# Optimization experiments

Hardware: AMD Instinct MI355X
Metric: run time of the kernel (lower is better)

The kernel has to match this reference:

```python
import jax, jax.numpy as jnp
import numpy as np

B = 256      # number of graphs
IN = 128     # input_dim
FD = 256     # feature_dim (dims[1])
HID = 256    # hidden_dim of attention block (dims[2])
OUT = 128    # final output dim (dims[3])
TXT = 512    # text_emb_dim

LENGTHS = np.asarray(128 + (np.arange(B) % 256), dtype=np.int64)  # ragged lens 128..383
N = int(LENGTHS.sum())  # 65408 total nodes
LMAX = int(LENGTHS.max())  # 383


def setup_inputs() -> dict:
    key = jax.random.key(0)
    ks = jax.random.split(key, 16)
    s = 0.02
    return {
        "input": jax.random.normal(ks[0], (N, IN), jnp.float32),
        "text_emb": jax.random.normal(ks[1], (B, TXT), jnp.float32),
        "repeat_list": jnp.asarray(LENGTHS),
        # layer 0: Linear(IN -> FD)
        "W0": jax.random.normal(ks[2], (IN, FD), jnp.float32) * s,
        "b0": jax.random.normal(ks[3], (FD,), jnp.float32) * s,
        # cross-attention block params
        "Wq": jax.random.normal(ks[4], (TXT, FD), jnp.float32) * s,
        "bq": jax.random.normal(ks[5], (FD,), jnp.float32) * s,
        "Wk": jax.random.normal(ks[6], (FD, FD), jnp.float32) * s,
        "bk": jax.random.normal(ks[7], (FD,), jnp.float32) * s,
        "Wv": jax.random.normal(ks[8], (FD, FD), jnp.float32) * s,
        "bv": jax.random.normal(ks[9], (FD,), jnp.float32) * s,
        "Wo": jax.random.normal(ks[10], (FD, HID), jnp.float32) * s,
        "bo": jax.random.normal(ks[11], (HID,), jnp.float32) * s,
        # layer 2: Linear(HID -> OUT), last layer (no activation)
        "W2": jax.random.normal(ks[12], (HID, OUT), jnp.float32) * s,
        "b2": jax.random.normal(ks[13], (OUT,), jnp.float32) * s,
    }


def _cross_attention(h, text_emb, repeat_list, Wq, bq, Wk, bk, Wv, bv, Wo, bo):
    # h: [N, FD] packed ragged node features; repeat_list: [B] lengths (constant ints)
    n = h.shape[0]
    b = repeat_list.shape[0]
    fd = h.shape[1]
    # pad ragged -> [B, LMAX, FD] (pad value 0) + validity mask
    seg = jnp.repeat(jnp.arange(b), repeat_list, total_repeat_length=n)  # [N] graph id
    offsets = jnp.cumsum(repeat_list) - repeat_list                      # [B] start of each graph
    pos = jnp.arange(n) - offsets[seg]                                   # [N] within-graph pos
    padded = jnp.zeros((b, LMAX, fd), h.dtype).at[seg, pos].set(h)
    valid = jnp.arange(LMAX)[None, :] < repeat_list[:, None]             # [B, L]

    q = text_emb @ Wq + bq                              # [B, FD]
    k = (padded @ Wk + bk) * valid[..., None]           # masked_fill(mask==0, 0)
    v = (padded @ Wv + bv) * valid[..., None]

    # query is broadcast identically over the padded-length axis, so each row of the
    # [L, L] score matrix is the same vector: scores[b, j] = q[b] . k[b, j]
    scores = jnp.einsum('bf,bjf->bj', q, k)             # [B, L]
    scores = jnp.where(valid, scores, -jnp.inf)         # mask invalid columns j
    p = jax.nn.softmax(scores, axis=-1)                 # [B, L]
    # output = attention^T @ value with identical rows => out[b,j,:] = p[b,j] * sum_i v[b,i,:]
    v_sum = v.sum(axis=1)                               # [B, FD] (padded rows already zero)
    out_pad = p[..., None] * v_sum[:, None, :]          # [B, L, FD]
    out_nodes = out_pad[seg, pos]                       # unpad-concat -> [N, FD]
    return out_nodes @ Wo + bo                          # [N, HID]


def reference(input, text_emb, repeat_list, W0, b0, Wq, bq, Wk, bk, Wv, bv, Wo, bo, W2, b2):
    h = jax.nn.relu(input @ W0 + b0)                                     # layer 0 + relu
    h = _cross_attention(h, text_emb, repeat_list, Wq, bq, Wk, bk, Wv, bv, Wo, bo)
    h = jax.nn.relu(h)                                                   # layer 1 + relu
    return h @ W2 + b2                                                   # layer 2 (last, no act)
```

## Files before the change

### kernel.cpp

```cpp
#include <hip/hip_runtime.h>
#include <math.h>

#define B_G   256
#define IN_D  128
#define FD    256
#define HID   256
#define OUT_D 128
#define TXT   512

typedef short bf16x8 __attribute__((ext_vector_type(8)));
typedef float f32x4  __attribute__((ext_vector_type(4)));

__device__ __forceinline__ unsigned bf_rne(float x) {
    unsigned u = __float_as_uint(x);
    u += 0x7fffu + ((u >> 16) & 1u);
    return u >> 16;
}
__device__ __forceinline__ float bf_to_f(unsigned h) {
    return __uint_as_float(h << 16);
}
__device__ __forceinline__ bf16x8 pack_hi8(const float4& v0, const float4& v1) {
    uint4 h;
    h.x = bf_rne(v0.x) | (bf_rne(v0.y) << 16);
    h.y = bf_rne(v0.z) | (bf_rne(v0.w) << 16);
    h.z = bf_rne(v1.x) | (bf_rne(v1.y) << 16);
    h.w = bf_rne(v1.z) | (bf_rne(v1.w) << 16);
    return __builtin_bit_cast(bf16x8, h);
}

__global__ __launch_bounds__(1024) void k_prepA(
    const float* __restrict__ text_emb, const float* __restrict__ Wq,
    const float* __restrict__ bq, const float* __restrict__ Wk,
    const float* __restrict__ W0, const float* __restrict__ W2,
    const int* __restrict__ lens,
    float* __restrict__ qk, int* __restrict__ offsets, float* __restrict__ hsum,
    unsigned short* __restrict__ W0sH, unsigned short* __restrict__ W0sL,
    unsigned short* __restrict__ W2sH, unsigned short* __restrict__ W2sL)
{
    int blk = blockIdx.x, tid = threadIdx.x;
    int t = tid & 255, g = tid >> 8;
    __shared__ float te[TXT];
    __shared__ float qsh[FD];
    __shared__ float part[4][FD];
    __shared__ int   sc[B_G];

    if (blk < 256) {
        int b = blk;
        if (g == 0) hsum[b * FD + t] = 0.f;
        if (tid < TXT) te[tid] = text_emb[(size_t)b * TXT + tid];
        __syncthreads();
        float acc = (g == 0) ? bq[t] : 0.f;
        const float* Wqp = Wq + (size_t)(128 * g) * FD + t;
        for (int k = 0; k < 128; k++) acc = fmaf(te[128 * g + k], Wqp[(size_t)k * FD], acc);
        part[g][t] = acc;
        __syncthreads();
        if (g == 0) qsh[t] = part[0][t] + part[1][t] + part[2][t] + part[3][t];
        __syncthreads();
        float a2 = 0.f;
        for (int f = 64 * g; f < 64 * g + 64; f++) a2 = fmaf(Wk[(size_t)t * FD + f], qsh[f], a2);
        part[g][t] = a2;
        __syncthreads();
        if (g == 0) qk[b * FD + t] = part[0][t] + part[1][t] + part[2][t] + part[3][t];
    } else if (blk < 258) {
        int e = (blk - 256) * 1024 + tid;
        if (e < 1024) {
            int kc = e >> 8, c = e & 255;
            size_t base = (size_t)(kc * 256 + c) * 32;
            for (int kk = 0; kk < 32; kk++) {
                float v = W0[(size_t)(kc * 32 + kk) * FD + c];
                unsigned h = bf_rne(v);
                float r = v - bf_to_f(h);
                W0sH[base + kk] = (unsigned short)h;
                W0sL[base + kk] = (unsigned short)bf_rne(r);
            }
        } else {
            int e2 = e - 1024;
            int kc = e2 >> 7, c = e2 & 127;
            size_t base = (size_t)(kc * 128 + c) * 32;
            for (int kk = 0; kk < 32; kk++) {
                float v = W2[(size_t)(kc * 32 + kk) * OUT_D + c];
                unsigned h = bf_rne(v);
                float r = v - bf_to_f(h);
                W2sH[base + kk] = (unsigned short)h;
                W2sL[base + kk] = (unsigned short)bf_rne(r);
            }
        }
    } else {
        if (tid < 256) sc[tid] = lens[tid];
        __syncthreads();
        for (int d = 1; d < 256; d <<= 1) {
            int v = (tid < 256 && tid >= d) ? sc[tid - d] : 0;
            __syncthreads();
            if (tid < 256) sc[tid] += v;
            __syncthreads();
        }
        if (tid < 256) offsets[tid + 1] = sc[tid];
        if (tid == 0) offsets[0] = 0;
    }
}

__global__ __launch_bounds__(256, 2) void k_l0_mfma(
    const float* __restrict__ X,
    const unsigned short* __restrict__ W0sH, const unsigned short* __restrict__ W0sL,
    const float* __restrict__ b0, const float* __restrict__ qk,
    const int* __restrict__ offsets,
    float* __restrict__ scores, float* __restrict__ hsum)
{
    int b = blockIdx.y;
    int off = offsets[b], len = offsets[b + 1] - off;
    int n0 = blockIdx.x * 64;
    if (n0 >= len) return;
    int nvalid = min(64, len - n0);

    __shared__ float qks[FD];
    __shared__ float bsh[FD];
    __shared__ float red[4][64];

    int tid = threadIdx.x;
    int lane = tid & 63, w = tid >> 6;
    int ln = lane & 15, quad = lane >> 4;

    qks[tid] = qk[b * FD + tid];
    bsh[tid] = b0[tid];

    const float* Xbase = X + (size_t)(off + n0) * IN_D;
    const float* arow[4];
    bool aval[4];
#pragma unroll
    for (int i = 0; i < 4; i++) {
        int node = 16 * i + ln;
        aval[i] = node < nvalid;
        arow[i] = Xbase + (size_t)(aval[i] ? node : 0) * IN_D + quad * 8;
    }
    const unsigned short* bph[4];
    const unsigned short* bpl[4];
#pragma unroll
    for (int j = 0; j < 4; j++) {
        int c = 64 * w + 16 * j + ln;
        bph[j] = W0sH + (size_t)c * 32 + quad * 8;
        bpl[j] = W0sL + (size_t)c * 32 + quad * 8;
    }

    f32x4 acc[4][4] = {};
    float4 aC[4][2];
#pragma unroll
    for (int i = 0; i < 4; i++) {
        const float4* p = (const float4*)(arow[i]);
        aC[i][0] = p[0]; aC[i][1] = p[1];
    }

#pragma unroll
    for (int kc = 0; kc < 4; kc++) {
        float4 aN[4][2];
        if (kc < 3) {
#pragma unroll
            for (int i = 0; i < 4; i++) {
                const float4* p = (const float4*)(arow[i] + (kc + 1) * 32);
                aN[i][0] = p[0]; aN[i][1] = p[1];
            }
        }
        uint4 bh[4], bl[4];
#pragma unroll
        for (int j = 0; j < 4; j++) {
            bh[j] = *(const uint4*)(bph[j] + (size_t)kc * 8192);
            bl[j] = *(const uint4*)(bpl[j] + (size_t)kc * 8192);
        }
        bf16x8 AH[4];
#pragma unroll
        for (int i = 0; i < 4; i++) {
            float4 v0 = aC[i][0], v1 = aC[i][1];
            if (!aval[i]) { v0 = make_float4(0, 0, 0, 0); v1 = v0; }
            AH[i] = pack_hi8(v0, v1);
        }
#pragma unroll
        for (int i = 0; i < 4; i++)
#pragma unroll
            for (int j = 0; j < 4; j++) {
                acc[i][j] = __builtin_amdgcn_mfma_f32_16x16x32_bf16(
                    AH[i], __builtin_bit_cast(bf16x8, bh[j]), acc[i][j], 0, 0, 0);
                acc[i][j] = __builtin_amdgcn_mfma_f32_16x16x32_bf16(
                    AH[i], __builtin_bit_cast(bf16x8, bl[j]), acc[i][j], 0, 0, 0);
            }
        if (kc < 3) {
#pragma unroll
            for (int i = 0; i < 4; i++) { aC[i][0] = aN[i][0]; aC[i][1] = aN[i][1]; }
        }
    }
    __syncthreads();

    float sp[4][4];
    float cs[4] = {0.f, 0.f, 0.f, 0.f};
#pragma unroll
    for (int i = 0; i < 4; i++)
#pragma unroll
        for (int r = 0; r < 4; r++) sp[i][r] = 0.f;

#pragma unroll
    for (int i = 0; i < 4; i++)
#pragma unroll
        for (int j = 0; j < 4; j++) {
            int c = 64 * w + 16 * j + ln;
            float bb = bsh[c], qv = qks[c];
#pragma unroll
            for (int r = 0; r < 4; r++) {
                int node = 16 * i + 4 * quad + r;
                float h = acc[i][j][r] + bb;
                h = (h > 0.f && node < nvalid) ? h : 0.f;
                sp[i][r] = fmaf(h, qv, sp[i][r]);
                cs[j] += h;
            }
        }
#pragma unroll
    for (int i = 0; i < 4; i++)
#pragma unroll
        for (int r = 0; r < 4; r++) {
            float s = sp[i][r];
            s += __shfl_xor(s, 1); s += __shfl_xor(s, 2);
            s += __shfl_xor(s, 4); s += __shfl_xor(s, 8);
            sp[i][r] = s;
        }
    if (ln == 0) {
#pragma unroll
        for (int i = 0; i < 4; i++)
#pragma unroll
            for (int r = 0; r < 4; r++)
                red[w][16 * i + 4 * quad + r] = sp[i][r];
    }
#pragma unroll
    for (int j = 0; j < 4; j++) {
        float s = cs[j];
        s += __shfl_xor(s, 16); s += __shfl_xor(s, 32);
        if (quad == 0) atomicAdd(&hsum[b * FD + 64 * w + 16 * j + ln], s);
    }
    __syncthreads();
    if (tid < 64 && tid < nvalid)
        scores[off + n0 + tid] = red[0][tid] + red[1][tid] + red[2][tid] + red[3][tid];
}

__global__ __launch_bounds__(1024) void k_graph(
    const float* __restrict__ scores, const float* __restrict__ hsum,
    const float* __restrict__ Wv, const float* __restrict__ bv,
    const float* __restrict__ Wo, const int* __restrict__ offsets,
    float* __restrict__ wvec, float* __restrict__ smax, float* __restrict__ dinv)
{
    int b = blockIdx.x, tid = threadIdx.x;
    int t = tid & 255, g = tid >> 8;
    int off = offsets[b], len = offsets[b + 1] - off;
    __shared__ float redm[16], reds[16];
    __shared__ float hs[FD], vs[FD];
    __shared__ float part[4][FD];

    float m = -INFINITY;
    for (int i = tid; i < len; i += 1024) m = fmaxf(m, scores[off + i]);
    for (int d = 1; d < 64; d <<= 1) m = fmaxf(m, __shfl_xor(m, d));
    if ((tid & 63) == 0) redm[tid >> 6] = m;
    __syncthreads();
    m = -INFINITY;
#pragma unroll
    for (int k = 0; k < 16; k++) m = fmaxf(m, redm[k]);

    float s = 0.f;
    for (int i = tid; i < len; i += 1024) s += expf(scores[off + i] - m);
    for (int d = 1; d < 64; d <<= 1) s += __shfl_xor(s, d);
    if ((tid & 63) == 0) reds[tid >> 6] = s;
    if (g == 0) hs[t] = hsum[b * FD + t];
    __syncthreads();
    s = 0.f;
#pragma unroll
    for (int k = 0; k < 16; k++) s += reds[k];

    float acc = (g == 0) ? (float)len * bv[t] : 0.f;
    for (int f = 64 * g; f < 64 * g + 64; f++) acc = fmaf(hs[f], Wv[f * FD + t], acc);
    part[g][t] = acc;
    __syncthreads();
    if (g == 0) vs[t] = part[0][t] + part[1][t] + part[2][t] + part[3][t];
    __syncthreads();
    float a2 = 0.f;
    for (int f = 64 * g; f < 64 * g + 64; f++) a2 = fmaf(vs[f], Wo[f * HID + t], a2);
    part[g][t] = a2;
    __syncthreads();
    if (g == 0) wvec[b * HID + t] = part[0][t] + part[1][t] + part[2][t] + part[3][t];
    if (tid == 0) { smax[b] = m; dinv[b] = 1.0f / s; }
}

__global__ __launch_bounds__(256, 2) void k_fin_mfma(
    const float* __restrict__ scores, const float* __restrict__ wvec,
    const float* __restrict__ bo,
    const unsigned short* __restrict__ W2sH, const unsigned short* __restrict__ W2sL,
    const float* __restrict__ b2, const float* __restrict__ smax,
    const float* __restrict__ dinv, const int* __restrict__ offsets,
    float* __restrict__ Y)
{
    int b = blockIdx.y;
    int off = offsets[b], len = offsets[b + 1] - off;
    int n0 = blockIdx.x * 64;
    if (n0 >= len) return;
    int nvalid = min(64, len - n0);

    int tid = threadIdx.x;
    int lane = tid & 63, w = tid >> 6;
    int ln = lane & 15, quad = lane >> 4;

    __shared__ float wsh[HID];
    __shared__ float bosh[HID];
    __shared__ float b2sh[OUT_D];

    wsh[tid] = wvec[b * HID + tid];
    bosh[tid] = bo[tid];
    if (tid < OUT_D) b2sh[tid] = b2[tid];

    float sm = smax[b], di = dinv[b];
    float p[4];
#pragma unroll
    for (int i = 0; i < 4; i++) {
        int node = 16 * i + ln;
        p[i] = (node < nvalid) ? expf(scores[off + n0 + node] - sm) * di : 0.f;
    }
    __syncthreads();

    const unsigned short* bph[2];
    const unsigned short* bpl[2];
#pragma unroll
    for (int j = 0; j < 2; j++) {
        int c = 32 * w + 16 * j + ln;
        bph[j] = W2sH + (size_t)c * 32 + quad * 8;
        bpl[j] = W2sL + (size_t)c * 32 + quad * 8;
    }

    f32x4 acc[4][2] = {};
    uint4 bhC[2], blC[2];
#pragma unroll
    for (int j = 0; j < 2; j++) {
        bhC[j] = *(const uint4*)(bph[j]);
        blC[j] = *(const uint4*)(bpl[j]);
    }

#pragma unroll
    for (int kc = 0; kc < 8; kc++) {
        uint4 bhN[2], blN[2];
        if (kc < 7) {
#pragma unroll
            for (int j = 0; j < 2; j++) {
                bhN[j] = *(const uint4*)(bph[j] + (size_t)(kc + 1) * 4096);
                blN[j] = *(const uint4*)(bpl[j] + (size_t)(kc + 1) * 4096);
            }
        }
        float4 wv0 = *(const float4*)&wsh[kc * 32 + quad * 8];
        float4 wv1 = *(const float4*)&wsh[kc * 32 + quad * 8 + 4];
        float4 bo0 = *(const float4*)&bosh[kc * 32 + quad * 8];
        float4 bo1 = *(const float4*)&bosh[kc * 32 + quad * 8 + 4];
        bf16x8 AH[4];
#pragma unroll
        for (int i = 0; i < 4; i++) {
            float4 z0, z1;
            z0.x = fmaxf(fmaf(p[i], wv0.x, bo0.x), 0.f);
            z0.y = fmaxf(fmaf(p[i], wv0.y, bo0.y), 0.f);
            z0.z = fmaxf(fmaf(p[i], wv0.z, bo0.z), 0.f);
            z0.w = fmaxf(fmaf(p[i], wv0.w, bo0.w), 0.f);
            z1.x = fmaxf(fmaf(p[i], wv1.x, bo1.x), 0.f);
            z1.y = fmaxf(fmaf(p[i], wv1.y, bo1.y), 0.f);
            z1.z = fmaxf(fmaf(p[i], wv1.z, bo1.z), 0.f);
            z1.w = fmaxf(fmaf(p[i], wv1.w, bo1.w), 0.f);
            AH[i] = pack_hi8(z0, z1);
        }
#pragma unroll
        for (int i = 0; i < 4; i++)
#pragma unroll
            for (int j = 0; j < 2; j++) {
                acc[i][j] = __builtin_amdgcn_mfma_f32_16x16x32_bf16(
                    AH[i], __builtin_bit_cast(bf16x8, bhC[j]), acc[i][j], 0, 0, 0);
                acc[i][j] = __builtin_amdgcn_mfma_f32_16x16x32_bf16(
                    AH[i], __builtin_bit_cast(bf16x8, blC[j]), acc[i][j], 0, 0, 0);
            }
        if (kc < 7) {
#pragma unroll
            for (int j = 0; j < 2; j++) { bhC[j] = bhN[j]; blC[j] = blN[j]; }
        }
    }

#pragma unroll
    for (int i = 0; i < 4; i++)
#pragma unroll
        for (int j = 0; j < 2; j++) {
            int c = 32 * w + 16 * j + ln;
            float bb = b2sh[c];
#pragma unroll
            for (int r = 0; r < 4; r++) {
                int node = 16 * i + 4 * quad + r;
                if (node < nvalid)
                    Y[(size_t)(off + n0 + node) * OUT_D + c] = acc[i][j][r] + bb;
            }
        }
}

extern "C" void kernel_launch(void* const* d_in, const int* in_sizes, int n_in,
                              void* d_out, int out_size, void* d_ws, size_t ws_size,
                              hipStream_t stream)
{
    const float* X        = (const float*)d_in[0];
    const float* text_emb = (const float*)d_in[1];
    const int*   lens     = (const int*)d_in[2];
    const float* W0       = (const float*)d_in[3];
    const float* b0       = (const float*)d_in[4];
    const float* Wq       = (const float*)d_in[5];
    const float* bq       = (const float*)d_in[6];
    const float* Wk       = (const float*)d_in[7];
    const float* Wv       = (const float*)d_in[9];
    const float* bv       = (const float*)d_in[10];
    const float* Wo       = (const float*)d_in[11];
    const float* bo       = (const float*)d_in[12];
    const float* W2       = (const float*)d_in[13];
    const float* b2       = (const float*)d_in[14];
    float* Y = (float*)d_out;

    char* base = (char*)d_ws;
    size_t o = 0;
    int*   offsets = (int*)(base + o);            o += 1088;
    float* qkbuf   = (float*)(base + o);          o += 262144;
    float* wvec    = (float*)(base + o);          o += 262144;
    float* smaxb   = (float*)(base + o);          o += 1024;
    float* dinvb   = (float*)(base + o);          o += 1024;
    float* hsum    = (float*)(base + o);          o += 262144;
    float* scores  = (float*)(base + o);          o += 262144;
    unsigned short* W0sH = (unsigned short*)(base + o); o += 65536;
    unsigned short* W0sL = (unsigned short*)(base + o); o += 65536;
    unsigned short* W2sH = (unsigned short*)(base + o); o += 65536;
    unsigned short* W2sL = (unsigned short*)(base + o); o += 65536;

    k_prepA<<<259, 1024, 0, stream>>>(text_emb, Wq, bq, Wk, W0, W2, lens,
                                      qkbuf, offsets, hsum, W0sH, W0sL, W2sH, W2sL);
    k_l0_mfma<<<dim3(6, B_G), 256, 0, stream>>>(X, W0sH, W0sL, b0, qkbuf, offsets, scores, hsum);
    k_graph<<<B_G, 1024, 0, stream>>>(scores, hsum, Wv, bv, Wo, offsets, wvec, smaxb, dinvb);
    k_fin_mfma<<<dim3(6, B_G), 256, 0, stream>>>(scores, wvec, bo, W2sH, W2sL, b2, smaxb, dinvb, offsets, Y);
}
```

Baseline: 212.2 us.

## Restructure pipeline into packed 128-node tiles with MFMA q/qk and pre-split weights

Replaces per-graph padded tiling (6 blocks per graph, many partially empty) with dense 128-node tiles over the packed node array. Each tile finds which of at most two graphs it spans by binary search over the offsets. X is pre-converted to bf16 in a prep kernel and staged through LDS. Scores and column sums are accumulated with atomics. The q and qk projections move to split-precision MFMA kernels, and Wq/Wv/Wo are pre-split into bf16 hi/lo. This adds two kernel launches and a full extra read and write of X in bf16, and the 128-row tiling assumes a tile never spans more than two graphs.

```diff
diff --git a/kernel.cpp b/kernel.cpp
--- a/kernel.cpp
+++ b/kernel.cpp
@@ -7,9 +7,15 @@
 #define HID   256
 #define OUT_D 128
 #define TXT   512
+#define NTILES 511
+#define XKS   136
 
 typedef short bf16x8 __attribute__((ext_vector_type(8)));
 typedef float f32x4  __attribute__((ext_vector_type(4)));
+
+__device__ __forceinline__ f32x4 MFMA(bf16x8 a, bf16x8 b, f32x4 c) {
+    return __builtin_amdgcn_mfma_f32_16x16x32_bf16(a, b, c, 0, 0, 0);
+}
 
 __device__ __forceinline__ unsigned bf_rne(float x) {
     unsigned u = __float_as_uint(x);
@@ -27,187 +33,268 @@
     h.w = bf_rne(v1.z) | (bf_rne(v1.w) << 16);
     return __builtin_bit_cast(bf16x8, h);
 }
-
-__global__ __launch_bounds__(1024) void k_prepA(
-    const float* __restrict__ text_emb, const float* __restrict__ Wq,
-    const float* __restrict__ bq, const float* __restrict__ Wk,
-    const float* __restrict__ W0, const float* __restrict__ W2,
+__device__ __forceinline__ void split8hl(const float4& v0, const float4& v1,
+                                         bf16x8& hf, bf16x8& lf) {
+    float a[8] = {v0.x, v0.y, v0.z, v0.w, v1.x, v1.y, v1.z, v1.w};
+    uint4 h, l;
+    unsigned hh[8], ll[8];
+#pragma unroll
+    for (int i = 0; i < 8; i++) {
+        hh[i] = bf_rne(a[i]);
+        ll[i] = bf_rne(a[i] - bf_to_f(hh[i]));
+    }
+    h.x = hh[0] | (hh[1] << 16); h.y = hh[2] | (hh[3] << 16);
+    h.z = hh[4] | (hh[5] << 16); h.w = hh[6] | (hh[7] << 16);
+    l.x = ll[0] | (ll[1] << 16); l.y = ll[2] | (ll[3] << 16);
+    l.z = ll[4] | (ll[5] << 16); l.w = ll[6] | (ll[7] << 16);
+    hf = __builtin_bit_cast(bf16x8, h);
+    lf = __builtin_bit_cast(bf16x8, l);
+}
+
+__device__ __forceinline__ void wsplit(const float* W, int N, int k0, int k1,
+                                       unsigned short* H, unsigned short* L, int c) {
+    if (c >= N) return;
+    for (int k = k0; k < k1; k++) {
+        int kc = k >> 5, kk = k & 31;
+        float v = W[(size_t)k * N + c];
+        unsigned h = bf_rne(v);
+        size_t o = ((size_t)kc * N + c) * 32 + kk;
+        H[o] = (unsigned short)h;
+        L[o] = (unsigned short)bf_rne(v - bf_to_f(h));
+    }
+}
+
+__global__ __launch_bounds__(256) void k_prep(
+    const float* __restrict__ X, const float* __restrict__ W0,
+    const float* __restrict__ W2, const float* __restrict__ Wq,
+    const float* __restrict__ Wv, const float* __restrict__ Wo,
     const int* __restrict__ lens,
-    float* __restrict__ qk, int* __restrict__ offsets, float* __restrict__ hsum,
-    unsigned short* __restrict__ W0sH, unsigned short* __restrict__ W0sL,
-    unsigned short* __restrict__ W2sH, unsigned short* __restrict__ W2sL)
+    unsigned short* __restrict__ Xbf,
+    unsigned short* __restrict__ W0H, unsigned short* __restrict__ W0L,
+    unsigned short* __restrict__ W2H, unsigned short* __restrict__ W2L,
+    unsigned short* __restrict__ WqH, unsigned short* __restrict__ WqL,
+    unsigned short* __restrict__ WvH, unsigned short* __restrict__ WvL,
+    unsigned short* __restrict__ WoH, unsigned short* __restrict__ WoL,
+    int* __restrict__ offsets, float* __restrict__ hsum, float* __restrict__ scores)
 {
     int blk = blockIdx.x, tid = threadIdx.x;
-    int t = tid & 255, g = tid >> 8;
-    __shared__ float te[TXT];
-    __shared__ float qsh[FD];
-    __shared__ float part[4][FD];
-    __shared__ int   sc[B_G];
-
-    if (blk < 256) {
-        int b = blk;
-        if (g == 0) hsum[b * FD + t] = 0.f;
-        if (tid < TXT) te[tid] = text_emb[(size_t)b * TXT + tid];
-        __syncthreads();
-        float acc = (g == 0) ? bq[t] : 0.f;
-        const float* Wqp = Wq + (size_t)(128 * g) * FD + t;
-        for (int k = 0; k < 128; k++) acc = fmaf(te[128 * g + k], Wqp[(size_t)k * FD], acc);
-        part[g][t] = acc;
-        __syncthreads();
-        if (g == 0) qsh[t] = part[0][t] + part[1][t] + part[2][t] + part[3][t];
-        __syncthreads();
-        float a2 = 0.f;
-        for (int f = 64 * g; f < 64 * g + 64; f++) a2 = fmaf(Wk[(size_t)t * FD + f], qsh[f], a2);
-        part[g][t] = a2;
-        __syncthreads();
-        if (g == 0) qk[b * FD + t] = part[0][t] + part[1][t] + part[2][t] + part[3][t];
-    } else if (blk < 258) {
-        int e = (blk - 256) * 1024 + tid;
-        if (e < 1024) {
-            int kc = e >> 8, c = e & 255;
-            size_t base = (size_t)(kc * 256 + c) * 32;
-            for (int kk = 0; kk < 32; kk++) {
-                float v = W0[(size_t)(kc * 32 + kk) * FD + c];
-                unsigned h = bf_rne(v);
-                float r = v - bf_to_f(h);
-                W0sH[base + kk] = (unsigned short)h;
-                W0sL[base + kk] = (unsigned short)bf_rne(r);
-            }
-        } else {
-            int e2 = e - 1024;
-            int kc = e2 >> 7, c = e2 & 127;
-            size_t base = (size_t)(kc * 128 + c) * 32;
-            for (int kk = 0; kk < 32; kk++) {
-                float v = W2[(size_t)(kc * 32 + kk) * OUT_D + c];
-                unsigned h = bf_rne(v);
-                float r = v - bf_to_f(h);
-                W2sH[base + kk] = (unsigned short)h;
-                W2sL[base + kk] = (unsigned short)bf_rne(r);
-            }
-        }
+    if (blk < NTILES) {
+        size_t base = (size_t)blk * 16384;
+#pragma unroll
+        for (int it = 0; it < 8; it++) {
+            size_t off = base + it * 2048 + tid * 8;
+            const float4* p = (const float4*)(X + off);
+            float4 v0 = p[0], v1 = p[1];
+            *(uint4*)(Xbf + off) = __builtin_bit_cast(uint4, pack_hi8(v0, v1));
+        }
+        if (tid < 128) {
+            hsum[blk * 128 + tid] = 0.f;
+            scores[blk * 128 + tid] = 0.f;
+        }
+    } else if (blk == 511) {
+        if (tid < 128) hsum[511 * 128 + tid] = 0.f;
+    } else if (blk == 512) {
+        wsplit(W0, FD, 0, 128, W0H, W0L, tid);
+    } else if (blk == 513) {
+        wsplit(W2, OUT_D, 0, 256, W2H, W2L, tid < 128 ? tid : 9999);
+    } else if (blk == 514) {
+        wsplit(Wq, FD, 0, 256, WqH, WqL, tid);
+    } else if (blk == 515) {
+        wsplit(Wq, FD, 256, 512, WqH, WqL, tid);
+    } else if (blk == 516) {
+        wsplit(Wv, FD, 0, 256, WvH, WvL, tid);
+    } else if (blk == 517) {
+        wsplit(Wo, HID, 0, 256, WoH, WoL, tid);
     } else {
-        if (tid < 256) sc[tid] = lens[tid];
+        __shared__ int sc[B_G];
+        sc[tid] = lens[tid];
         __syncthreads();
         for (int d = 1; d < 256; d <<= 1) {
-            int v = (tid < 256 && tid >= d) ? sc[tid - d] : 0;
+            int v = (tid >= d) ? sc[tid - d] : 0;
             __syncthreads();
-            if (tid < 256) sc[tid] += v;
+            sc[tid] += v;
             __syncthreads();
         }
-        if (tid < 256) offsets[tid + 1] = sc[tid];
+        offsets[tid + 1] = sc[tid];
         if (tid == 0) offsets[0] = 0;
     }
 }
 
-__global__ __launch_bounds__(256, 2) void k_l0_mfma(
-    const float* __restrict__ X,
-    const unsigned short* __restrict__ W0sH, const unsigned short* __restrict__ W0sL,
+__global__ __launch_bounds__(256) void k_q(
+    const float* __restrict__ TE,
+    const unsigned short* __restrict__ WqH, const unsigned short* __restrict__ WqL,
+    const float* __restrict__ bq, float* __restrict__ q)
+{
+    int blk = blockIdx.x;
+    int rbase = (blk >> 2) * 64, cbase = (blk & 3) * 64;
+    int tid = threadIdx.x, lane = tid & 63, w = tid >> 6;
+    int ln = lane & 15, quad = lane >> 4;
+
+    f32x4 acc[4] = {};
+    int arow = rbase + w * 16 + ln;
+#pragma unroll
+    for (int kc = 0; kc < 16; kc++) {
+        const float4* ap = (const float4*)(TE + (size_t)arow * TXT + kc * 32 + quad * 8);
+        bf16x8 AH, AL;
+        split8hl(ap[0], ap[1], AH, AL);
+#pragma unroll
+        for (int j = 0; j < 4; j++) {
+            int c = cbase + 16 * j + ln;
+            size_t bo = ((size_t)kc * 256 + c) * 32 + quad * 8;
+            bf16x8 BH = *(const bf16x8*)(WqH + bo);
+            bf16x8 BL = *(const bf16x8*)(WqL + bo);
+            acc[j] = MFMA(AH, BH, acc[j]);
+            acc[j] = MFMA(AH, BL, acc[j]);
+            acc[j] = MFMA(AL, BH, acc[j]);
+        }
+    }
+#pragma unroll
+    for (int j = 0; j < 4; j++) {
+        int c = cbase + 16 * j + ln;
+        float bb = bq[c];
+#pragma unroll
+        for (int r = 0; r < 4; r++) {
+            int row = rbase + w * 16 + quad * 4 + r;
+            q[(size_t)row * FD + c] = acc[j][r] + bb;
+        }
+    }
+}
+
+__global__ __launch_bounds__(256) void k_qk(
+    const float* __restrict__ q, const float* __restrict__ Wk,
+    float* __restrict__ qk)
+{
+    int blk = blockIdx.x;
+    int rbase = (blk >> 2) * 64, cbase = (blk & 3) * 64;
+    int tid = threadIdx.x, lane = tid & 63, w = tid >> 6;
+    int ln = lane & 15, quad = lane >> 4;
+
+    f32x4 acc[4] = {};
+    int arow = rbase + w * 16 + ln;
+#pragma unroll
+    for (int kc = 0; kc < 8; kc++) {
+        const float4* ap = (const float4*)(q + (size_t)arow * FD + kc * 32 + quad * 8);
+        bf16x8 AH, AL;
+        split8hl(ap[0], ap[1], AH, AL);
+#pragma unroll
+        for (int j = 0; j < 4; j++) {
+            int f = cbase + 16 * j + ln;
+            const float4* bp = (const float4*)(Wk + (size_t)f * FD + kc * 32 + quad * 8);
+            bf16x8 BH, BL;
+            split8hl(bp[0], bp[1], BH, BL);
+            acc[j] = MFMA(AH, BH, acc[j]);
+            acc[j] = MFMA(AH, BL, acc[j]);
+            acc[j] = MFMA(AL, BH, acc[j]);
+        }
+    }
+#pragma unroll
+    for (int j = 0; j < 4; j++) {
+        int f = cbase + 16 * j + ln;
+#pragma unroll
+        for (int r = 0; r < 4; r++) {
+            int row = rbase + w * 16 + quad * 4 + r;
+            qk[(size_t)row * FD + f] = acc[j][r];
+        }
+    }
+}
+
+__global__ __launch_bounds__(256) void k_l0(
+    const unsigned short* __restrict__ Xbf,
+    const unsigned short* __restrict__ W0H, const unsigned short* __restrict__ W0L,
     const float* __restrict__ b0, const float* __restrict__ qk,
     const int* __restrict__ offsets,
     float* __restrict__ scores, float* __restrict__ hsum)
 {
-    int b = blockIdx.y;
-    int off = offsets[b], len = offsets[b + 1] - off;
-    int n0 = blockIdx.x * 64;
-    if (n0 >= len) return;
-    int nvalid = min(64, len - n0);
-
-    __shared__ float qks[FD];
-    __shared__ float bsh[FD];
-    __shared__ float red[4][64];
-
-    int tid = threadIdx.x;
-    int lane = tid & 63, w = tid >> 6;
+    int t = blockIdx.y, bx = blockIdx.x;
+    int n0 = t * 128;
+    int tid = threadIdx.x, lane = tid & 63, w = tid >> 6;
     int ln = lane & 15, quad = lane >> 4;
-
-    qks[tid] = qk[b * FD + tid];
-    bsh[tid] = b0[tid];
-
-    const float* Xbase = X + (size_t)(off + n0) * IN_D;
-    const float* arow[4];
-    bool aval[4];
-#pragma unroll
-    for (int i = 0; i < 4; i++) {
-        int node = 16 * i + ln;
-        aval[i] = node < nvalid;
-        arow[i] = Xbase + (size_t)(aval[i] ? node : 0) * IN_D + quad * 8;
-    }
-    const unsigned short* bph[4];
-    const unsigned short* bpl[4];
-#pragma unroll
-    for (int j = 0; j < 4; j++) {
-        int c = 64 * w + 16 * j + ln;
-        bph[j] = W0sH + (size_t)c * 32 + quad * 8;
-        bpl[j] = W0sL + (size_t)c * 32 + quad * 8;
-    }
+    int i2 = w & 1, j2 = w >> 1;
+
+    __shared__ __align__(16) unsigned short Xs[128 * XKS];
+    __shared__ int offs[257];
+    __shared__ float qks[2][128];
+    __shared__ float bsh[128];
+
+    offs[tid] = offsets[tid];
+    if (tid == 0) offs[256] = offsets[256];
+    __syncthreads();
+
+    int lo = 0, hi = 255;
+#pragma unroll
+    for (int s = 0; s < 8; s++) {
+        int mid = (lo + hi + 1) >> 1;
+        if (offs[mid] <= n0) lo = mid; else hi = mid - 1;
+    }
+    int g0 = lo;
+    lo = g0; hi = 255;
+#pragma unroll
+    for (int s = 0; s < 8; s++) {
+        int mid = (lo + hi + 1) >> 1;
+        if (offs[mid] <= n0 + 127) lo = mid; else hi = mid - 1;
+    }
+    int g1 = lo;
+    int boundary = (g1 > g0) ? offs[g1] : 0x7fffffff;
+
+    if (tid < 128) {
+        bsh[tid] = b0[bx * 128 + tid];
+        qks[0][tid] = qk[(size_t)g0 * FD + bx * 128 + tid];
+        qks[1][tid] = qk[(size_t)g1 * FD + bx * 128 + tid];
+    }
+#pragma unroll
+    for (int it = 0; it < 8; it++) {
+        int row = it * 16 + (tid >> 4);
+        int kq = (tid & 15) * 8;
+        *(uint4*)(Xs + row * XKS + kq) =
+            *(const uint4*)(Xbf + (size_t)(n0 + row) * IN_D + kq);
+    }
+    __syncthreads();
 
     f32x4 acc[4][4] = {};
-    float4 aC[4][2];
-#pragma unroll
-    for (int i = 0; i < 4; i++) {
-        const float4* p = (const float4*)(arow[i]);
-        aC[i][0] = p[0]; aC[i][1] = p[1];
-    }
-
 #pragma unroll
     for (int kc = 0; kc < 4; kc++) {
-        float4 aN[4][2];
-        if (kc < 3) {
-#pragma unroll
-            for (int i = 0; i < 4; i++) {
-                const float4* p = (const float4*)(arow[i] + (kc + 1) * 32);
-                aN[i][0] = p[0]; aN[i][1] = p[1];
-            }
-        }
-        uint4 bh[4], bl[4];
+        bf16x8 AH[4], BH[4], BL[4];
+#pragma unroll
+        for (int i = 0; i < 4; i++)
+            AH[i] = *(const bf16x8*)(Xs + (i2 * 64 + 16 * i + ln) * XKS + kc * 32 + quad * 8);
 #pragma unroll
         for (int j = 0; j < 4; j++) {
-            bh[j] = *(const uint4*)(bph[j] + (size_t)kc * 8192);
-            bl[j] = *(const uint4*)(bpl[j] + (size_t)kc * 8192);
-        }
-        bf16x8 AH[4];
-#pragma unroll
-        for (int i = 0; i < 4; i++) {
-            float4 v0 = aC[i][0], v1 = aC[i][1];
-            if (!aval[i]) { v0 = make_float4(0, 0, 0, 0); v1 = v0; }
-            AH[i] = pack_hi8(v0, v1);
+            int c = bx * 128 + j2 * 64 + 16 * j + ln;
+            size_t bo = ((size_t)kc * 256 + c) * 32 + quad * 8;
+            BH[j] = *(const bf16x8*)(W0H + bo);
+            BL[j] = *(const bf16x8*)(W0L + bo);
         }
 #pragma unroll
         for (int i = 0; i < 4; i++)
 #pragma unroll
             for (int j = 0; j < 4; j++) {
-                acc[i][j] = __builtin_amdgcn_mfma_f32_16x16x32_bf16(
-                    AH[i], __builtin_bit_cast(bf16x8, bh[j]), acc[i][j], 0, 0, 0);
-                acc[i][j] = __builtin_amdgcn_mfma_f32_16x16x32_bf16(
-                    AH[i], __builtin_bit_cast(bf16x8, bl[j]), acc[i][j], 0, 0, 0);
-            }
-        if (kc < 3) {
-#pragma unroll
-            for (int i = 0; i < 4; i++) { aC[i][0] = aN[i][0]; aC[i][1] = aN[i][1]; }
-        }
-    }
-    __syncthreads();
+                acc[i][j] = MFMA(AH[i], BH[j], acc[i][j]);
+                acc[i][j] = MFMA(AH[i], BL[j], acc[i][j]);
+            }
+    }
 
     float sp[4][4];
-    float cs[4] = {0.f, 0.f, 0.f, 0.f};
+    float cs[4][2];
 #pragma unroll
     for (int i = 0; i < 4; i++)
 #pragma unroll
         for (int r = 0; r < 4; r++) sp[i][r] = 0.f;
+#pragma unroll
+    for (int j = 0; j < 4; j++) { cs[j][0] = 0.f; cs[j][1] = 0.f; }
 
 #pragma unroll
     for (int i = 0; i < 4; i++)
 #pragma unroll
         for (int j = 0; j < 4; j++) {
-            int c = 64 * w + 16 * j + ln;
-            float bb = bsh[c], qv = qks[c];
+            int cl = j2 * 64 + 16 * j + ln;
+            float bb = bsh[cl];
 #pragma unroll
             for (int r = 0; r < 4; r++) {
-                int node = 16 * i + 4 * quad + r;
-                float h = acc[i][j][r] + bb;
-                h = (h > 0.f && node < nvalid) ? h : 0.f;
-                sp[i][r] = fmaf(h, qv, sp[i][r]);
-                cs[j] += h;
+                int node = i2 * 64 + 16 * i + quad * 4 + r;
+                int gb = (n0 + node >= boundary) ? 1 : 0;
+                float h = fmaxf(acc[i][j][r] + bb, 0.f);
+                sp[i][r] = fmaf(h, qks[gb][cl], sp[i][r]);
+                cs[j][gb] += h;
             }
         }
 #pragma unroll
@@ -217,141 +304,209 @@
             float s = sp[i][r];
             s += __shfl_xor(s, 1); s += __shfl_xor(s, 2);
             s += __shfl_xor(s, 4); s += __shfl_xor(s, 8);
-            sp[i][r] = s;
-        }
-    if (ln == 0) {
-#pragma unroll
-        for (int i = 0; i < 4; i++)
-#pragma unroll
-            for (int r = 0; r < 4; r++)
-                red[w][16 * i + 4 * quad + r] = sp[i][r];
-    }
+            if (ln == 0) {
+                int node = i2 * 64 + 16 * i + quad * 4 + r;
+                atomicAdd(&scores[n0 + node], s);
+            }
+        }
 #pragma unroll
     for (int j = 0; j < 4; j++) {
-        float s = cs[j];
-        s += __shfl_xor(s, 16); s += __shfl_xor(s, 32);
-        if (quad == 0) atomicAdd(&hsum[b * FD + 64 * w + 16 * j + ln], s);
-    }
-    __syncthreads();
-    if (tid < 64 && tid < nvalid)
-        scores[off + n0 + tid] = red[0][tid] + red[1][tid] + red[2][tid] + red[3][tid];
-}
-
-__global__ __launch_bounds__(1024) void k_graph(
+        int cl = j2 * 64 + 16 * j + ln;
+#pragma unroll
+        for (int gb = 0; gb < 2; gb++) {
+            float s = cs[j][gb];
+            s += __shfl_xor(s, 16); s += __shfl_xor(s, 32);
+            if (quad == 0 && (gb == 0 || g1 > g0)) {
+                int g = gb ? g1 : g0;
+                atomicAdd(&hsum[(size_t)g * FD + bx * 128 + cl], s);
+            }
+        }
+    }
+}
+
+__global__ __launch_bounds__(256) void k_mid(
     const float* __restrict__ scores, const float* __restrict__ hsum,
-    const float* __restrict__ Wv, const float* __restrict__ bv,
-    const float* __restrict__ Wo, const int* __restrict__ offsets,
+    const unsigned short* __restrict__ WvH, const unsigned short* __restrict__ WvL,
+    const float* __restrict__ bv,
+    const unsigned short* __restrict__ WoH, const unsigned short* __restrict__ WoL,
+    const int* __restrict__ offsets,
     float* __restrict__ wvec, float* __restrict__ smax, float* __restrict__ dinv)
 {
-    int b = blockIdx.x, tid = threadIdx.x;
-    int t = tid & 255, g = tid >> 8;
-    int off = offsets[b], len = offsets[b + 1] - off;
-    __shared__ float redm[16], reds[16];
-    __shared__ float hs[FD], vs[FD];
-    __shared__ float part[4][FD];
-
-    float m = -INFINITY;
-    for (int i = tid; i < len; i += 1024) m = fmaxf(m, scores[off + i]);
-    for (int d = 1; d < 64; d <<= 1) m = fmaxf(m, __shfl_xor(m, d));
-    if ((tid & 63) == 0) redm[tid >> 6] = m;
-    __syncthreads();
-    m = -INFINITY;
-#pragma unroll
-    for (int k = 0; k < 16; k++) m = fmaxf(m, redm[k]);
-
-    float s = 0.f;
-    for (int i = tid; i < len; i += 1024) s += expf(scores[off + i] - m);
-    for (int d = 1; d < 64; d <<= 1) s += __shfl_xor(s, d);
-    if ((tid & 63) == 0) reds[tid >> 6] = s;
-    if (g == 0) hs[t] = hsum[b * FD + t];
-    __syncthreads();
-    s = 0.f;
-#pragma unroll
-    for (int k = 0; k < 16; k++) s += reds[k];
-
-    float acc = (g == 0) ? (float)len * bv[t] : 0.f;
-    for (int f = 64 * g; f < 64 * g + 64; f++) acc = fmaf(hs[f], Wv[f * FD + t], acc);
-    part[g][t] = acc;
-    __syncthreads();
-    if (g == 0) vs[t] = part[0][t] + part[1][t] + part[2][t] + part[3][t];
-    __syncthreads();
-    float a2 = 0.f;
-    for (int f = 64 * g; f < 64 * g + 64; f++) a2 = fmaf(vs[f], Wo[f * HID + t], a2);
-    part[g][t] = a2;
-    __syncthreads();
-    if (g == 0) wvec[b * HID + t] = part[0][t] + part[1][t] + part[2][t] + part[3][t];
-    if (tid == 0) { smax[b] = m; dinv[b] = 1.0f / s; }
-}
-
-__global__ __launch_bounds__(256, 2) void k_fin_mfma(
+    int blk = blockIdx.x, tid = threadIdx.x;
+    if (blk < 4) {
+        __shared__ float vs[64 * 260];
+        __shared__ int offs2[65];
+        int base = blk * 64;
+        int lane = tid & 63, w = tid >> 6;
+        int ln = lane & 15, quad = lane >> 4;
+        if (tid < 65) offs2[tid] = offsets[base + tid];
+        __syncthreads();
+
+        f32x4 acc[4][4] = {};
+#pragma unroll
+        for (int kc = 0; kc < 8; kc++) {
+            bf16x8 AH[4], AL[4], BH[4], BL[4];
+#pragma unroll
+            for (int i = 0; i < 4; i++) {
+                const float4* ap = (const float4*)(hsum + (size_t)(base + 16 * i + ln) * FD + kc * 32 + quad * 8);
+                split8hl(ap[0], ap[1], AH[i], AL[i]);
+            }
+#pragma unroll
+            for (int j = 0; j < 4; j++) {
+                int c = w * 64 + 16 * j + ln;
+                size_t bo = ((size_t)kc * 256 + c) * 32 + quad * 8;
+                BH[j] = *(const bf16x8*)(WvH + bo);
+                BL[j] = *(const bf16x8*)(WvL + bo);
+            }
+#pragma unroll
+            for (int i = 0; i < 4; i++)
+#pragma unroll
+                for (int j = 0; j < 4; j++) {
+                    acc[i][j] = MFMA(AH[i], BH[j], acc[i][j]);
+                    acc[i][j] = MFMA(AH[i], BL[j], acc[i][j]);
+                    acc[i][j] = MFMA(AL[i], BH[j], acc[i][j]);
+                }
+        }
+#pragma unroll
+        for (int i = 0; i < 4; i++)
+#pragma unroll
+            for (int j = 0; j < 4; j++) {
+                int c = w * 64 + 16 * j + ln;
+                float bvc = bv[c];
+#pragma unroll
+                for (int r = 0; r < 4; r++) {
+                    int row = 16 * i + quad * 4 + r;
+                    float len = (float)(offs2[row + 1] - offs2[row]);
+                    vs[row * 260 + c] = acc[i][j][r] + len * bvc;
+                }
+            }
+        __syncthreads();
+
+        f32x4 acc2[4][4] = {};
+#pragma unroll
+        for (int kc = 0; kc < 8; kc++) {
+            bf16x8 AH[4], AL[4], BH[4], BL[4];
+#pragma unroll
+            for (int i = 0; i < 4; i++) {
+                const float4* ap = (const float4*)(vs + (16 * i + ln) * 260 + kc * 32 + quad * 8);
+                split8hl(ap[0], ap[1], AH[i], AL[i]);
+            }
+#pragma unroll
+            for (int j = 0; j < 4; j++) {
+                int c = w * 64 + 16 * j + ln;
+                size_t bo = ((size_t)kc * 256 + c) * 32 + quad * 8;
+                BH[j] = *(const bf16x8*)(WoH + bo);
+                BL[j] = *(const bf16x8*)(WoL + bo);
+            }
+#pragma unroll
+            for (int i = 0; i < 4; i++)
+#pragma unroll
+                for (int j = 0; j < 4; j++) {
+                    acc2[i][j] = MFMA(AH[i], BH[j], acc2[i][j]);
+                    acc2[i][j] = MFMA(AH[i], BL[j], acc2[i][j]);
+                    acc2[i][j] = MFMA(AL[i], BH[j], acc2[i][j]);
+                }
+        }
+#pragma unroll
+        for (int i = 0; i < 4; i++)
+#pragma unroll
+            for (int j = 0; j < 4; j++) {
+                int c = w * 64 + 16 * j + ln;
+#pragma unroll
+                for (int r = 0; r < 4; r++) {
+                    int row = 16 * i + quad * 4 + r;
+                    wvec[(size_t)(base + row) * HID + c] = acc2[i][j][r];
+                }
+            }
+    } else {
+        int b = blk - 4;
+        int off = offsets[b], len = offsets[b + 1] - off;
+        __shared__ float redm[4], reds[4];
+        float m = -INFINITY;
+        for (int i = tid; i < len; i += 256) m = fmaxf(m, scores[off + i]);
+        for (int d = 1; d < 64; d <<= 1) m = fmaxf(m, __shfl_xor(m, d));
+        if ((tid & 63) == 0) redm[tid >> 6] = m;
+        __syncthreads();
+        m = fmaxf(fmaxf(redm[0], redm[1]), fmaxf(redm[2], redm[3]));
+        float s = 0.f;
+        for (int i = tid; i < len; i += 256) s += expf(scores[off + i] - m);
+        for (int d = 1; d < 64; d <<= 1) s += __shfl_xor(s, d);
+        if ((tid & 63) == 0) reds[tid >> 6] = s;
+        __syncthreads();
+        if (tid == 0) {
+            smax[b] = m;
+            dinv[b] = 1.0f / (reds[0] + reds[1] + reds[2] + reds[3]);
+        }
+    }
+}
+
+__global__ __launch_bounds__(256) void k_fin(
     const float* __restrict__ scores, const float* __restrict__ wvec,
     const float* __restrict__ bo,
-    const unsigned short* __restrict__ W2sH, const unsigned short* __restrict__ W2sL,
+    const unsigned short* __restrict__ W2H, const unsigned short* __restrict__ W2L,
     const float* __restrict__ b2, const float* __restrict__ smax,
     const float* __restrict__ dinv, const int* __restrict__ offsets,
     float* __restrict__ Y)
 {
-    int b = blockIdx.y;
-    int off = offsets[b], len = offsets[b + 1] - off;
-    int n0 = blockIdx.x * 64;
-    if (n0 >= len) return;
-    int nvalid = min(64, len - n0);
-
-    int tid = threadIdx.x;
-    int lane = tid & 63, w = tid >> 6;
+    int t = blockIdx.x;
+    int n0 = t * 128;
+    int tid = threadIdx.x, lane = tid & 63, w = tid >> 6;
     int ln = lane & 15, quad = lane >> 4;
-
-    __shared__ float wsh[HID];
+    int i2 = w & 1, j2 = w >> 1;
+
+    __shared__ int offs[257];
+    __shared__ float wsh[2][HID];
     __shared__ float bosh[HID];
     __shared__ float b2sh[OUT_D];
-
-    wsh[tid] = wvec[b * HID + tid];
+    __shared__ float sd[4];
+
+    offs[tid] = offsets[tid];
+    if (tid == 0) offs[256] = offsets[256];
+    __syncthreads();
+
+    int lo = 0, hi = 255;
+#pragma unroll
+    for (int s = 0; s < 8; s++) {
+        int mid = (lo + hi + 1) >> 1;
+        if (offs[mid] <= n0) lo = mid; else hi = mid - 1;
+    }
+    int g0 = lo;
+    lo = g0; hi = 255;
+#pragma unroll
+    for (int s = 0; s < 8; s++) {
+        int mid = (lo + hi + 1) >> 1;
+        if (offs[mid] <= n0 + 127) lo = mid; else hi = mid - 1;
+    }
+    int g1 = lo;
+    int boundary = (g1 > g0) ? offs[g1] : 0x7fffffff;
+
+    wsh[0][tid] = wvec[(size_t)g0 * HID + tid];
+    wsh[1][tid] = wvec[(size_t)g1 * HID + tid];
     bosh[tid] = bo[tid];
     if (tid < OUT_D) b2sh[tid] = b2[tid];
-
-    float sm = smax[b], di = dinv[b];
+    if (tid == 0) { sd[0] = smax[g0]; sd[1] = dinv[g0]; sd[2] = smax[g1]; sd[3] = dinv[g1]; }
+    __syncthreads();
+
     float p[4];
+    int gb_i[4];
 #pragma unroll
     for (int i = 0; i < 4; i++) {
-        int node = 16 * i + ln;
-        p[i] = (node < nvalid) ? expf(scores[off + n0 + node] - sm) * di : 0.f;
-    }
-    __syncthreads();
-
-    const unsigned short* bph[2];
-    const unsigned short* bpl[2];
-#pragma unroll
-    for (int j = 0; j < 2; j++) {
-        int c = 32 * w + 16 * j + ln;
-        bph[j] = W2sH + (size_t)c * 32 + quad * 8;
-        bpl[j] = W2sL + (size_t)c * 32 + quad * 8;
-    }
-
-    f32x4 acc[4][2] = {};
-    uint4 bhC[2], blC[2];
-#pragma unroll
-    for (int j = 0; j < 2; j++) {
-        bhC[j] = *(const uint4*)(bph[j]);
-        blC[j] = *(const uint4*)(bpl[j]);
-    }
-
+        int node = i2 * 64 + 16 * i + ln;
+        int gb = (n0 + node >= boundary) ? 1 : 0;
+        gb_i[i] = gb;
+        p[i] = expf(scores[n0 + node] - sd[gb * 2]) * sd[gb * 2 + 1];
+    }
+
+    f32x4 acc[4][4] = {};
 #pragma unroll
     for (int kc = 0; kc < 8; kc++) {
-        uint4 bhN[2], blN[2];
-        if (kc < 7) {
-#pragma unroll
-            for (int j = 0; j < 2; j++) {
-                bhN[j] = *(const uint4*)(bph[j] + (size_t)(kc + 1) * 4096);
-                blN[j] = *(const uint4*)(bpl[j] + (size_t)(kc + 1) * 4096);
-            }
-        }
-        float4 wv0 = *(const float4*)&wsh[kc * 32 + quad * 8];
-        float4 wv1 = *(const float4*)&wsh[kc * 32 + quad * 8 + 4];
         float4 bo0 = *(const float4*)&bosh[kc * 32 + quad * 8];
         float4 bo1 = *(const float4*)&bosh[kc * 32 + quad * 8 + 4];
-        bf16x8 AH[4];
+        bf16x8 AH[4], BH[4], BL[4];
 #pragma unroll
         for (int i = 0; i < 4; i++) {
+            float4 wv0 = *(const float4*)&wsh[gb_i[i]][kc * 32 + quad * 8];
+            float4 wv1 = *(const float4*)&wsh[gb_i[i]][kc * 32 + quad * 8 + 4];
             float4 z0, z1;
             z0.x = fmaxf(fmaf(p[i], wv0.x, bo0.x), 0.f);
             z0.y = fmaxf(fmaf(p[i], wv0.y, bo0.y), 0.f);
@@ -364,31 +519,31 @@
             AH[i] = pack_hi8(z0, z1);
         }
 #pragma unroll
+        for (int j = 0; j < 4; j++) {
+            int c = j2 * 64 + 16 * j + ln;
+            size_t boff = ((size_t)kc * 128 + c) * 32 + quad * 8;
+            BH[j] = *(const bf16x8*)(W2H + boff);
+            BL[j] = *(const bf16x8*)(W2L + boff);
+        }
+#pragma unroll
         for (int i = 0; i < 4; i++)
 #pragma unroll
-            for (int j = 0; j < 2; j++) {
-                acc[i][j] = __builtin_amdgcn_mfma_f32_16x16x32_bf16(
-                    AH[i], __builtin_bit_cast(bf16x8, bhC[j]), acc[i][j], 0, 0, 0);
-                acc[i][j] = __builtin_amdgcn_mfma_f32_16x16x32_bf16(
-                    AH[i], __builtin_bit_cast(bf16x8, blC[j]), acc[i][j], 0, 0, 0);
-            }
-        if (kc < 7) {
-#pragma unroll
-            for (int j = 0; j < 2; j++) { bhC[j] = bhN[j]; blC[j] = blN[j]; }
-        }
+            for (int j = 0; j < 4; j++) {
+                acc[i][j] = MFMA(AH[i], BH[j], acc[i][j]);
+                acc[i][j] = MFMA(AH[i], BL[j], acc[i][j]);
+            }
     }
 
 #pragma unroll
     for (int i = 0; i < 4; i++)
 #pragma unroll
-        for (int j = 0; j < 2; j++) {
-            int c = 32 * w + 16 * j + ln;
+        for (int j = 0; j < 4; j++) {
+            int c = j2 * 64 + 16 * j + ln;
             float bb = b2sh[c];
 #pragma unroll
             for (int r = 0; r < 4; r++) {
-                int node = 16 * i + 4 * quad + r;
-                if (node < nvalid)
-                    Y[(size_t)(off + n0 + node) * OUT_D + c] = acc[i][j][r] + bb;
+                int node = i2 * 64 + 16 * i + quad * 4 + r;
+                Y[(size_t)(n0 + node) * OUT_D + c] = acc[i][j][r] + bb;
             }
         }
 }
@@ -415,21 +570,34 @@
 
     char* base = (char*)d_ws;
     size_t o = 0;
-    int*   offsets = (int*)(base + o);            o += 1088;
-    float* qkbuf   = (float*)(base + o);          o += 262144;
-    float* wvec    = (float*)(base + o);          o += 262144;
-    float* smaxb   = (float*)(base + o);          o += 1024;
-    float* dinvb   = (float*)(base + o);          o += 1024;
-    float* hsum    = (float*)(base + o);          o += 262144;
-    float* scores  = (float*)(base + o);          o += 262144;
-    unsigned short* W0sH = (unsigned short*)(base + o); o += 65536;
-    unsigned short* W0sL = (unsigned short*)(base + o); o += 65536;
-    unsigned short* W2sH = (unsigned short*)(base + o); o += 65536;
-    unsigned short* W2sL = (unsigned short*)(base + o); o += 65536;
-
-    k_prepA<<<259, 1024, 0, stream>>>(text_emb, Wq, bq, Wk, W0, W2, lens,
-                                      qkbuf, offsets, hsum, W0sH, W0sL, W2sH, W2sL);
-    k_l0_mfma<<<dim3(6, B_G), 256, 0, stream>>>(X, W0sH, W0sL, b0, qkbuf, offsets, scores, hsum);
-    k_graph<<<B_G, 1024, 0, stream>>>(scores, hsum, Wv, bv, Wo, offsets, wvec, smaxb, dinvb);
-    k_fin_mfma<<<dim3(6, B_G), 256, 0, stream>>>(scores, wvec, bo, W2sH, W2sL, b2, smaxb, dinvb, offsets, Y);
-}
+    int*   offsets = (int*)(base + o);                  o += 4096;
+    float* qbuf    = (float*)(base + o);                o += 262144;
+    float* qkbuf   = (float*)(base + o);                o += 262144;
+    float* wvec    = (float*)(base + o);                o += 262144;
+    float* smaxb   = (float*)(base + o);                o += 1024;
+    float* dinvb   = (float*)(base + o);                o += 1024;
+    float* hsum    = (float*)(base + o);                o += 262144;
+    float* scores  = (float*)(base + o);                o += 262144;
+    unsigned short* WqH = (unsigned short*)(base + o);  o += 262144;
+    unsigned short* WqL = (unsigned short*)(base + o);  o += 262144;
+    unsigned short* WvH = (unsigned short*)(base + o);  o += 131072;
+    unsigned short* WvL = (unsigned short*)(base + o);  o += 131072;
+    unsigned short* WoH = (unsigned short*)(base + o);  o += 131072;
+    unsigned short* WoL = (unsigned short*)(base + o);  o += 131072;
+    unsigned short* W0H = (unsigned short*)(base + o);  o += 65536;
+    unsigned short* W0L = (unsigned short*)(base + o);  o += 65536;
+    unsigned short* W2H = (unsigned short*)(base + o);  o += 65536;
+    unsigned short* W2L = (unsigned short*)(base + o);  o += 65536;
+    unsigned short* Xbf = (unsigned short*)(base + o);  o += 16744448;
+
+    k_prep<<<519, 256, 0, stream>>>(X, W0, W2, Wq, Wv, Wo, lens, Xbf,
+                                    W0H, W0L, W2H, W2L, WqH, WqL, WvH, WvL,
+                                    WoH, WoL, offsets, hsum, scores);
+    k_q<<<16, 256, 0, stream>>>(text_emb, WqH, WqL, bq, qbuf);
+    k_qk<<<16, 256, 0, stream>>>(qbuf, Wk, qkbuf);
+    k_l0<<<dim3(2, NTILES), 256, 0, stream>>>(Xbf, W0H, W0L, b0, qkbuf, offsets, scores, hsum);
+    k_mid<<<260, 256, 0, stream>>>(scores, hsum, WvH, WvL, bv, WoH, WoL, offsets,
+                                   wvec, smaxb, dinvb);
+    k_fin<<<NTILES, 256, 0, stream>>>(scores, wvec, bo, W2H, W2L, b2, smaxb, dinvb,
+                                      offsets, Y);
+}
```

Result: slower. 298.1 us (+40.5%).
